# Performance work log

Measured on AMD Instinct MI355X. Metric: run time of the kernel, lower is better.

The kernel has to match this reference:

```python
import jax, jax.numpy as jnp
import numpy as np

N = 8192
D = 512
N_SLICE = 64
K = 8
H = 30 * K  # 240


def _gen_k_slice(rng):
    xx = rng.normal(0.0, 1.0, (N_SLICE, K, D))
    slices = np.zeros((N_SLICE, K, D), dtype=np.float64)
    for i in range(N_SLICE):
        _, _, vh = np.linalg.svd(xx[i], full_matrices=False)
        slices[i] = vh
    return slices.astype(np.float32)


def setup_inputs() -> dict:
    key = jax.random.key(0)
    k1, k2, k3, k4, k5, k6, k7 = jax.random.split(key, 7)
    rng = np.random.default_rng(0)
    # conv weights: PyTorch Conv1d default init ~ U(-s, s), s = 1/sqrt(fan_in)
    s1 = 1.0 / np.sqrt(K)
    s3 = 1.0 / np.sqrt(H)
    return {
        "X": jax.random.normal(k1, (N, D), dtype=jnp.float32),
        "Y": jax.random.normal(k2, (N, D), dtype=jnp.float32),
        "X_noise": jax.random.normal(k3, (N, N_SLICE * K), dtype=jnp.float32),
        "thetas": jnp.asarray(_gen_k_slice(rng)),                     # [S, K, D]
        "W1": jax.random.uniform(k4, (N_SLICE, H, K), jnp.float32, -s1, s1),
        "b1": jax.random.uniform(k5, (N_SLICE, H), jnp.float32, -s1, s1),
        "W3": jax.random.uniform(k6, (N_SLICE, H), jnp.float32, -s3, s3),
        "b3": jax.random.uniform(k7, (N_SLICE,), jnp.float32, -s3, s3),
        "sigma_noise": 0,
    }


def _mlp(sample, W1, b1, W3, b3):
    # sample: [N, S, K] -> grouped 1x1 conv k->H, relu, grouped conv H->1
    h1 = jax.nn.relu(jnp.einsum('nsk,shk->nsh', sample, W1) + b1[None])
    return jnp.einsum('nsh,sh->ns', h1, W3) + b3[None]  # [N, S]


def reference(X, Y, X_noise, thetas, W1, b1, W3, b3, sigma_noise):
    # batched per-slice projections (fuses the n_slice matmul loop)
    x_sample = jnp.einsum('nd,skd->nsk', X, thetas)  # [N, S, K]
    y_sample = jnp.einsum('nd,skd->nsk', Y, thetas)
    if sigma_noise > 0:
        x_sample = x_sample + sigma_noise * X_noise.reshape(X.shape[0], N_SLICE, K)
    pred_x = _mlp(x_sample, W1, b1, W3, b3)  # [N, S]
    pred_y = _mlp(y_sample, W1, b1, W3, b3)
    n_y = pred_y.shape[0]
    ret = jnp.mean(pred_x, axis=0) - jax.nn.logsumexp(
        pred_y - jnp.log(jnp.float32(n_y)), axis=0)
    return jnp.mean(-ret)
```

## Files before the change

kernel.cpp:

```cpp
#include <hip/hip_runtime.h>
#include <hip/hip_bf16.h>

#define NROWS 8192
#define DDIM  512
#define NS    64
#define KK    8
#define HH    240
#define SP    136
#define ARGN  2048
#define STG   6144
#define BWOFF 8704

typedef __attribute__((ext_vector_type(8))) _Float16 f16x8;
typedef __attribute__((ext_vector_type(4))) _Float16 f16x4;
typedef __attribute__((ext_vector_type(4))) float f32x4;

typedef __attribute__((address_space(3))) void       lds_void;
typedef const __attribute__((address_space(1))) void gbl_cvoid;

__device__ inline unsigned pk2u(float a, float b) {
    auto h = __builtin_amdgcn_cvt_pkrtz(a, b);
    unsigned u;
    __builtin_memcpy(&u, &h, sizeof(u));
    return u;
}

__device__ inline f16x4 pk4(float a, float b, float c, float d) {
    uint2 u = make_uint2(pk2u(a, b), pk2u(c, d));
    f16x4 r;
    __builtin_memcpy(&r, &u, sizeof(r));
    return r;
}

__device__ inline void gl16(const ushort* g, ushort* l) {
    __builtin_amdgcn_global_load_lds((gbl_cvoid*)g, (lds_void*)l, 16, 0, 0);
}

#define XN (NROWS * DDIM)
__global__ __launch_bounds__(256)
void pack_kernel(const float* __restrict__ X, const float* __restrict__ Y,
                 const float* __restrict__ Th, const float* __restrict__ W1,
                 const float* __restrict__ b1, const float* __restrict__ W3,
                 ushort* __restrict__ Xh, ushort* __restrict__ Yh,
                 ushort* __restrict__ Thh, ushort* __restrict__ W1h,
                 ushort* __restrict__ bwh)
{
    int t = blockIdx.x * 256 + threadIdx.x;
    int i = t * 4;
    if (i < 2 * XN + 262144 + 122880) {
        const float* src; ushort* dst; int off;
        if (i < XN)               { src = X;  dst = Xh;  off = i; }
        else if (i < 2 * XN)      { src = Y;  dst = Yh;  off = i - XN; }
        else if (i < 2 * XN + 262144) { src = Th; dst = Thh; off = i - 2 * XN; }
        else                      { src = W1; dst = W1h; off = i - (2 * XN + 262144); }
        float4 v = *(const float4*)(src + off);
        *(uint2*)(dst + off) = make_uint2(pk2u(v.x, v.y), pk2u(v.z, v.w));
    } else {
        int j = t - 2193408;
        int s = j / 60, r = j % 60;
        int src = s * HH + (r >> 2) * 16 + (r & 3) * 4;
        float4 b4 = *(const float4*)(b1 + src);
        float4 w4 = *(const float4*)(W3 + src);
        uint4 o = make_uint4(pk2u(b4.x, b4.y), pk2u(b4.z, b4.w),
                             pk2u(w4.x, w4.y), pk2u(w4.z, w4.w));
        *(uint4*)(bwh + j * 8) = o;
    }
}

__global__ __launch_bounds__(256, 4)
void proj_mlp_kernel(const ushort* __restrict__ Xh,
                     const ushort* __restrict__ Yh,
                     const float* __restrict__ Xn,
                     const ushort* __restrict__ Thh,
                     const ushort* __restrict__ W1h,
                     const ushort* __restrict__ bwh,
                     const float* __restrict__ sig_p,
                     float* __restrict__ sumx,
                     float* __restrict__ maxy,
                     float* __restrict__ sey)
{
    __shared__ __align__(16) ushort smem[16384];
    ushort* sl = smem;

    const int tid  = threadIdx.x;
    const int w    = __builtin_amdgcn_readfirstlane(tid >> 6);
    const int lane = tid & 63;
    const int bx   = blockIdx.x;
    const int by   = blockIdx.y;

    const bool isX = (bx < 128);
    const int  bxl = isX ? bx : (bx - 128);
    const ushort* srcA = (isX ? Xh : Yh) + (size_t)bxl * 64 * DDIM;
    const ushort* srcB = Thh + (size_t)by * 128 * DDIM;

    const int grow = (w << 4) + (lane >> 2);
    const int gchk = (lane & 3) ^ ((grow >> 1) & 3);
    const ushort* gA  = srcA + (size_t)grow * DDIM + gchk * 8;
    const ushort* gB0 = srcB + (size_t)grow * DDIM + gchk * 8;
    const ushort* gB1 = srcB + (size_t)(grow + 64) * DDIM + gchk * 8;
    const int woff = w * 512;

#define ISSUE(kf, st) { const int k_ = (kf) * 32; ushort* s_ = smem + (st); \
    gl16(gA  + k_, s_ + woff); \
    gl16(gB0 + k_, s_ + ARGN + woff); \
    gl16(gB1 + k_, s_ + ARGN + 2048 + woff); }

    f32x4 acc[2][4];
#pragma unroll
    for (int m = 0; m < 2; ++m)
#pragma unroll
        for (int n = 0; n < 4; ++n) acc[m][n] = (f32x4){0.f, 0.f, 0.f, 0.f};

    const int wr  = (w >> 1) * 32;
    const int wc  = (w & 1) * 64;
    const int r16 = lane & 15;
    const int hi4 = lane >> 4;

    int offA[2], offB[4];
#pragma unroll
    for (int m = 0; m < 2; ++m) {
        int row = wr + m * 16 + r16;
        offA[m] = row * 32 + ((hi4 ^ ((row >> 1) & 3)) * 8);
    }
#pragma unroll
    for (int n = 0; n < 4; ++n) {
        int row = wc + n * 16 + r16;
        offB[n] = ARGN + row * 32 + ((hi4 ^ ((row >> 1) & 3)) * 8);
    }

    ISSUE(0, 0);

#pragma unroll
    for (int kt = 0; kt < 16; ++kt) {
        asm volatile("s_waitcnt vmcnt(0)\n\ts_barrier" ::: "memory");

        if (kt < 15) ISSUE(kt + 1, ((kt + 1) & 1) * STG);

        const int cur = (kt & 1) * STG;
        f16x8 af[2], bfv[4];
#pragma unroll
        for (int m = 0; m < 2; ++m) af[m]  = *(const f16x8*)(smem + cur + offA[m]);
#pragma unroll
        for (int n = 0; n < 4; ++n) bfv[n] = *(const f16x8*)(smem + cur + offB[n]);
#pragma unroll
        for (int m = 0; m < 2; ++m)
#pragma unroll
            for (int n = 0; n < 4; ++n)
                acc[m][n] = __builtin_amdgcn_mfma_f32_16x16x32_f16(
                    af[m], bfv[n], acc[m][n], 0, 0, 0);
    }
    __syncthreads();

    {
        const ushort* g = bwh + (size_t)by * 7680;
#pragma unroll
        for (int r = 0; r < 4; ++r) {
            const int ch = r * 256 + w * 64;
            gl16(g + (size_t)(ch + lane) * 8, smem + BWOFF + ch * 8);
        }
    }

    const float sig = *sig_p;
    const bool addnoise = (sig > 0.f) && isX;
    const int n0g = bxl * 64;

#pragma unroll
    for (int m = 0; m < 2; ++m)
#pragma unroll
        for (int n = 0; n < 4; ++n) {
            const int col  = wc + n * 16 + r16;
            const int rowb = wr + m * 16 + hi4 * 4;
            float v[4];
#pragma unroll
            for (int j = 0; j < 4; ++j) {
                v[j] = acc[m][n][j];
                if (addnoise)
                    v[j] = fmaf(sig, Xn[(size_t)(n0g + rowb + j) * (NS * KK) + by * 128 + col], v[j]);
            }
            unsigned u01 = pk2u(v[0], v[1]);
            unsigned u23 = pk2u(v[2], v[3]);
            sl[(rowb + 0) * SP + col] = (ushort)u01;
            sl[(rowb + 1) * SP + col] = (ushort)(u01 >> 16);
            sl[(rowb + 2) * SP + col] = (ushort)u23;
            sl[(rowb + 3) * SP + col] = (ushort)(u23 >> 16);
        }
    asm volatile("s_waitcnt vmcnt(0)" ::: "memory");
    __syncthreads();

#pragma unroll 1
    for (int si = 0; si < 4; ++si) {
        const int sloc = w * 4 + si;
        const int s    = by * 16 + sloc;

        f16x4 bsamp[4];
#pragma unroll
        for (int nt = 0; nt < 4; ++nt) {
            f16x4 t = {0, 0, 0, 0};
            if (hi4 < 2)
                t = *(const f16x4*)(sl + (nt * 16 + r16) * SP + sloc * 8 + hi4 * 4);
            bsamp[nt] = t;
        }

        const ushort* w1p = W1h + (size_t)s * HH * KK;

        f32x4 acc2[4];
#pragma unroll
        for (int nt = 0; nt < 4; ++nt) acc2[nt] = (f32x4){0.f, 0.f, 0.f, 0.f};

#pragma unroll 5
        for (int ht = 0; ht < HH / 16; ++ht) {
            f16x4 aw = {0, 0, 0, 0};
            if (hi4 < 2)
                aw = *(const f16x4*)(w1p + (ht * 16 + r16) * 8 + hi4 * 4);
            f16x8 bw = *(const f16x8*)(smem + BWOFF + ((sloc * 15 + ht) * 4 + hi4) * 8);
            f32x4 z = (f32x4){(float)bw[0], (float)bw[1], (float)bw[2], (float)bw[3]};
            f16x4 w3f = {bw[4], bw[5], bw[6], bw[7]};
#pragma unroll
            for (int nt = 0; nt < 4; ++nt) {
                f32x4 t = __builtin_amdgcn_mfma_f32_16x16x16f16(aw, bsamp[nt], z, 0, 0, 0);
                f16x4 tb = pk4(fmaxf(t[0], 0.f), fmaxf(t[1], 0.f),
                               fmaxf(t[2], 0.f), fmaxf(t[3], 0.f));
                acc2[nt] = __builtin_amdgcn_mfma_f32_16x16x16f16(w3f, tb, acc2[nt], 0, 0, 0);
            }
        }

        if (isX) {
            float lsum = acc2[0][0] + acc2[1][0] + acc2[2][0] + acc2[3][0];
            lsum += __shfl_xor(lsum, 1);
            lsum += __shfl_xor(lsum, 2);
            lsum += __shfl_xor(lsum, 4);
            lsum += __shfl_xor(lsum, 8);
            if (lane == 0) sumx[s * 128 + bxl] = lsum;
        } else {
            float p[4];
#pragma unroll
            for (int nt = 0; nt < 4; ++nt) p[nt] = acc2[nt][0];
            float M = fmaxf(fmaxf(p[0], p[1]), fmaxf(p[2], p[3]));
            float se = __expf(p[0] - M) + __expf(p[1] - M)
                     + __expf(p[2] - M) + __expf(p[3] - M);
#pragma unroll
            for (int off = 1; off < 16; off <<= 1) {
                float Mo = __shfl_xor(M, off);
                float so = __shfl_xor(se, off);
                float Mm = fmaxf(M, Mo);
                se = se * __expf(M - Mm) + so * __expf(Mo - Mm);
                M = Mm;
            }
            if (lane == 0) {
                maxy[s * 128 + bxl] = M;
                sey[s * 128 + bxl]  = se;
            }
        }
    }
}

__global__ __launch_bounds__(256)
void final_kernel(const float* __restrict__ sumx,
                  const float* __restrict__ maxy,
                  const float* __restrict__ sey,
                  float* __restrict__ out)
{
    __shared__ float term_s[NS];
    const int tid = threadIdx.x;
    const int s = tid >> 2, q = tid & 3;
    const int base = s * 128 + q * 32;

    float sum = 0.f, M = -3.4e38f;
#pragma unroll 8
    for (int i = 0; i < 32; ++i) {
        sum += sumx[base + i];
        M = fmaxf(M, maxy[base + i]);
    }
    float se = 0.f;
#pragma unroll 8
    for (int i = 0; i < 32; ++i)
        se += sey[base + i] * __expf(maxy[base + i] - M);

#pragma unroll
    for (int off = 1; off < 4; off <<= 1) {
        float Mo = __shfl_xor(M, off);
        float so = __shfl_xor(se, off);
        float su = __shfl_xor(sum, off);
        float Mm = fmaxf(M, Mo);
        se = se * __expf(M - Mm) + so * __expf(Mo - Mm);
        M = Mm;
        sum += su;
    }
    if (q == 0)
        term_s[s] = M + logf(se) - logf((float)NROWS) - sum * (1.0f / (float)NROWS);
    __syncthreads();
    if (tid < 64) {
        float v = term_s[tid];
#pragma unroll
        for (int off = 1; off < 64; off <<= 1) v += __shfl_xor(v, off);
        if (tid == 0) out[0] = v * (1.0f / (float)NS);
    }
}

extern "C" void kernel_launch(void* const* d_in, const int* in_sizes, int n_in,
                              void* d_out, int out_size, void* d_ws, size_t ws_size,
                              hipStream_t stream)
{
    const float* X   = (const float*)d_in[0];
    const float* Y   = (const float*)d_in[1];
    const float* Xn  = (const float*)d_in[2];
    const float* Th  = (const float*)d_in[3];
    const float* W1  = (const float*)d_in[4];
    const float* b1  = (const float*)d_in[5];
    const float* W3  = (const float*)d_in[6];
    const float* sig = (const float*)d_in[8];

    ushort* Xh   = (ushort*)d_ws;
    ushort* Yh   = Xh + XN;
    ushort* Thh  = Yh + XN;
    ushort* W1h  = Thh + 262144;
    ushort* bwh  = W1h + 122880;
    float*  sumx = (float*)(bwh + 61440);
    float*  maxy = sumx + NS * 128;
    float*  sey  = maxy + NS * 128;

    pack_kernel<<<8583, 256, 0, stream>>>(X, Y, Th, W1, b1, W3,
                                          Xh, Yh, Thh, W1h, bwh);

    dim3 g1(256, 4, 1);
    proj_mlp_kernel<<<g1, 256, 0, stream>>>(Xh, Yh, Xn, Thh, W1h, bwh,
                                            sig, sumx, maxy, sey);
    final_kernel<<<1, 256, 0, stream>>>(sumx, maxy, sey, (float*)d_out);
}
```

Before: 66.83 us.

## Fuse X/Y fp16 conversion into projection kernel, loading fp32 directly to LDS

Stops pre-converting X and Y to fp16 in the pack kernel. The projection GEMM now streams fp32 tiles of X/Y straight into LDS with a new swizzled layout and converts them to fp16 in registers before the MFMA. This removes a full read and write of two 8192x512 arrays plus an extra pass over them. In exchange the GEMM moves twice as many A-operand bytes per tile, uses more LDS per stage, and does conversion work inside the inner loop.

```diff
diff --git a/kernel.cpp b/kernel.cpp
--- a/kernel.cpp
+++ b/kernel.cpp
@@ -7,8 +7,8 @@
 #define KK    8
 #define HH    240
 #define SP    136
-#define ARGN  2048
-#define STG   6144
+#define BOFFU 4096
+#define STGU  8192
 #define BWOFF 8704
 
 typedef __attribute__((ext_vector_type(8))) _Float16 f16x8;
@@ -35,28 +35,27 @@
 __device__ inline void gl16(const ushort* g, ushort* l) {
     __builtin_amdgcn_global_load_lds((gbl_cvoid*)g, (lds_void*)l, 16, 0, 0);
 }
-
-#define XN (NROWS * DDIM)
+__device__ inline void glf(const float* g, ushort* l) {
+    __builtin_amdgcn_global_load_lds((gbl_cvoid*)g, (lds_void*)l, 16, 0, 0);
+}
+
 __global__ __launch_bounds__(256)
-void pack_kernel(const float* __restrict__ X, const float* __restrict__ Y,
-                 const float* __restrict__ Th, const float* __restrict__ W1,
+void pack_kernel(const float* __restrict__ Th, const float* __restrict__ W1,
                  const float* __restrict__ b1, const float* __restrict__ W3,
-                 ushort* __restrict__ Xh, ushort* __restrict__ Yh,
                  ushort* __restrict__ Thh, ushort* __restrict__ W1h,
                  ushort* __restrict__ bwh)
 {
     int t = blockIdx.x * 256 + threadIdx.x;
-    int i = t * 4;
-    if (i < 2 * XN + 262144 + 122880) {
-        const float* src; ushort* dst; int off;
-        if (i < XN)               { src = X;  dst = Xh;  off = i; }
-        else if (i < 2 * XN)      { src = Y;  dst = Yh;  off = i - XN; }
-        else if (i < 2 * XN + 262144) { src = Th; dst = Thh; off = i - 2 * XN; }
-        else                      { src = W1; dst = W1h; off = i - (2 * XN + 262144); }
-        float4 v = *(const float4*)(src + off);
-        *(uint2*)(dst + off) = make_uint2(pk2u(v.x, v.y), pk2u(v.z, v.w));
+    if (t < 65536) {
+        int i = t * 4;
+        float4 v = *(const float4*)(Th + i);
+        *(uint2*)(Thh + i) = make_uint2(pk2u(v.x, v.y), pk2u(v.z, v.w));
+    } else if (t < 96256) {
+        int i = (t - 65536) * 4;
+        float4 v = *(const float4*)(W1 + i);
+        *(uint2*)(W1h + i) = make_uint2(pk2u(v.x, v.y), pk2u(v.z, v.w));
     } else {
-        int j = t - 2193408;
+        int j = t - 96256;
         int s = j / 60, r = j % 60;
         int src = s * HH + (r >> 2) * 16 + (r & 3) * 4;
         float4 b4 = *(const float4*)(b1 + src);
@@ -68,8 +67,8 @@
 }
 
 __global__ __launch_bounds__(256, 4)
-void proj_mlp_kernel(const ushort* __restrict__ Xh,
-                     const ushort* __restrict__ Yh,
+void proj_mlp_kernel(const float* __restrict__ X,
+                     const float* __restrict__ Y,
                      const float* __restrict__ Xn,
                      const ushort* __restrict__ Thh,
                      const ushort* __restrict__ W1h,
@@ -90,20 +89,25 @@
 
     const bool isX = (bx < 128);
     const int  bxl = isX ? bx : (bx - 128);
-    const ushort* srcA = (isX ? Xh : Yh) + (size_t)bxl * 64 * DDIM;
+    const float*  srcA = (isX ? X : Y) + (size_t)bxl * 64 * DDIM;
     const ushort* srcB = Thh + (size_t)by * 128 * DDIM;
+
+    const int arow = (w << 4) + (lane >> 2);
+    const int arsw = (lane >> 2) & 7;
+    const float* gA0 = srcA + (size_t)arow * DDIM + (((lane & 3) + 0) ^ arsw) * 4;
+    const float* gA1 = srcA + (size_t)arow * DDIM + (((lane & 3) + 4) ^ arsw) * 4;
 
     const int grow = (w << 4) + (lane >> 2);
     const int gchk = (lane & 3) ^ ((grow >> 1) & 3);
-    const ushort* gA  = srcA + (size_t)grow * DDIM + gchk * 8;
     const ushort* gB0 = srcB + (size_t)grow * DDIM + gchk * 8;
     const ushort* gB1 = srcB + (size_t)(grow + 64) * DDIM + gchk * 8;
     const int woff = w * 512;
 
-#define ISSUE(kf, st) { const int k_ = (kf) * 32; ushort* s_ = smem + (st); \
-    gl16(gA  + k_, s_ + woff); \
-    gl16(gB0 + k_, s_ + ARGN + woff); \
-    gl16(gB1 + k_, s_ + ARGN + 2048 + woff); }
+#define ISSUE(kf, stU) { const int k_ = (kf) * 32; ushort* s_ = smem + (stU); \
+    glf(gA0 + k_, s_ + w * 1024); \
+    glf(gA1 + k_, s_ + w * 1024 + 512); \
+    gl16(gB0 + k_, s_ + BOFFU + woff); \
+    gl16(gB1 + k_, s_ + BOFFU + 2048 + woff); }
 
     f32x4 acc[2][4];
 #pragma unroll
@@ -116,16 +120,23 @@
     const int r16 = lane & 15;
     const int hi4 = lane >> 4;
 
-    int offA[2], offB[4];
+    int offA32[2][2];
 #pragma unroll
     for (int m = 0; m < 2; ++m) {
         int row = wr + m * 16 + r16;
-        offA[m] = row * 32 + ((hi4 ^ ((row >> 1) & 3)) * 8);
-    }
+        int rsw = row & 7;
+#pragma unroll
+        for (int cc = 0; cc < 2; ++cc) {
+            int p = (hi4 * 2 + cc) ^ rsw;
+            offA32[m][cc] = (row >> 4) * 2048 + (p >> 2) * 1024
+                          + (row & 15) * 64 + (p & 3) * 16;
+        }
+    }
+    int offB[4];
 #pragma unroll
     for (int n = 0; n < 4; ++n) {
         int row = wc + n * 16 + r16;
-        offB[n] = ARGN + row * 32 + ((hi4 ^ ((row >> 1) & 3)) * 8);
+        offB[n] = BOFFU + row * 32 + ((hi4 ^ ((row >> 1) & 3)) * 8);
     }
 
     ISSUE(0, 0);
@@ -134,14 +145,22 @@
     for (int kt = 0; kt < 16; ++kt) {
         asm volatile("s_waitcnt vmcnt(0)\n\ts_barrier" ::: "memory");
 
-        if (kt < 15) ISSUE(kt + 1, ((kt + 1) & 1) * STG);
-
-        const int cur = (kt & 1) * STG;
+        if (kt < 15) ISSUE(kt + 1, ((kt + 1) & 1) * STGU);
+
+        const int curU = (kt & 1) * STGU;
+        const char* curB = (const char*)smem + (kt & 1) * 16384;
+
         f16x8 af[2], bfv[4];
 #pragma unroll
-        for (int m = 0; m < 2; ++m) af[m]  = *(const f16x8*)(smem + cur + offA[m]);
-#pragma unroll
-        for (int n = 0; n < 4; ++n) bfv[n] = *(const f16x8*)(smem + cur + offB[n]);
+        for (int m = 0; m < 2; ++m) {
+            f32x4 lo = *(const f32x4*)(curB + offA32[m][0]);
+            f32x4 hi = *(const f32x4*)(curB + offA32[m][1]);
+            uint4 u = make_uint4(pk2u(lo[0], lo[1]), pk2u(lo[2], lo[3]),
+                                 pk2u(hi[0], hi[1]), pk2u(hi[2], hi[3]));
+            __builtin_memcpy(&af[m], &u, 16);
+        }
+#pragma unroll
+        for (int n = 0; n < 4; ++n) bfv[n] = *(const f16x8*)(smem + curU + offB[n]);
 #pragma unroll
         for (int m = 0; m < 2; ++m)
 #pragma unroll
@@ -310,20 +329,17 @@
     const float* W3  = (const float*)d_in[6];
     const float* sig = (const float*)d_in[8];
 
-    ushort* Xh   = (ushort*)d_ws;
-    ushort* Yh   = Xh + XN;
-    ushort* Thh  = Yh + XN;
+    ushort* Thh  = (ushort*)d_ws;
     ushort* W1h  = Thh + 262144;
     ushort* bwh  = W1h + 122880;
     float*  sumx = (float*)(bwh + 61440);
     float*  maxy = sumx + NS * 128;
     float*  sey  = maxy + NS * 128;
 
-    pack_kernel<<<8583, 256, 0, stream>>>(X, Y, Th, W1, b1, W3,
-                                          Xh, Yh, Thh, W1h, bwh);
+    pack_kernel<<<391, 256, 0, stream>>>(Th, W1, b1, W3, Thh, W1h, bwh);
 
     dim3 g1(256, 4, 1);
-    proj_mlp_kernel<<<g1, 256, 0, stream>>>(Xh, Yh, Xn, Thh, W1h, bwh,
+    proj_mlp_kernel<<<g1, 256, 0, stream>>>(X, Y, Xn, Thh, W1h, bwh,
                                             sig, sumx, maxy, sey);
     final_kernel<<<1, 256, 0, stream>>>(sumx, maxy, sey, (float*)d_out);
 }
```

Result: no change. 66.10 us (-1.1%).
